# Performance work log

Measured on AMD Instinct MI355X. Metric: run time of the kernel, lower is better.

Reference implementation:

```python
import jax, jax.numpy as jnp
import numpy as np


def _cell(xt, h, c, Wih, Whh, b):
    # Single LSTM cell step; PyTorch gate order i, f, g, o.
    g = xt @ Wih.T + h @ Whh.T + b
    i, f, gg, o = jnp.split(g, 4, axis=-1)
    c = jax.nn.sigmoid(f) * c + jax.nn.sigmoid(i) * jnp.tanh(gg)
    h = jax.nn.sigmoid(o) * jnp.tanh(c)
    return h, c


def _lstm_layer(x, Wih, Whh, b):
    # x: [B, T, D] -> hs: [B, T, H], (h, c): final states [B, H]
    B = x.shape[0]
    H = Whh.shape[1]
    h0 = jnp.zeros((B, H), x.dtype)
    c0 = jnp.zeros((B, H), x.dtype)

    def step(carry, xt):
        h, c = carry
        h, c = _cell(xt, h, c, Wih, Whh, b)
        return (h, c), h

    (h, c), hs = jax.lax.scan(step, (h0, c0), jnp.swapaxes(x, 0, 1))
    return jnp.swapaxes(hs, 0, 1), h, c


def setup_inputs() -> dict:
    key = jax.random.key(0)
    B, T_SRC, D_IN, H, TGT = 512, 256, 32, 128, 64
    ks = iter(jax.random.split(key, 32))
    s_in = 1.0 / np.sqrt(H)

    def u(k, shape):
        return jax.random.uniform(k, shape, jnp.float32, -s_in, s_in)

    inp = {"x": jax.random.normal(next(ks), (B, T_SRC, D_IN), jnp.float32),
           "target_len": TGT}
    for pre in ("enc", "dec"):
        for l, din in ((0, D_IN), (1, H)):
            inp[f"{pre}_Wih{l}"] = u(next(ks), (4 * H, din))
            inp[f"{pre}_Whh{l}"] = u(next(ks), (4 * H, H))
            inp[f"{pre}_bih{l}"] = u(next(ks), (4 * H,))
            inp[f"{pre}_bhh{l}"] = u(next(ks), (4 * H,))
    inp["lin_W"] = u(next(ks), (D_IN, H))
    inp["lin_b"] = u(next(ks), (D_IN,))
    return inp


def reference(x, target_len,
              enc_Wih0, enc_Whh0, enc_bih0, enc_bhh0,
              enc_Wih1, enc_Whh1, enc_bih1, enc_bhh1,
              dec_Wih0, dec_Whh0, dec_bih0, dec_bhh0,
              dec_Wih1, dec_Whh1, dec_bih1, dec_bhh1,
              lin_W, lin_b):
    # --- encoder: 2-layer full-sequence LSTM, zero initial state ---
    hs0, eh0, ec0 = _lstm_layer(x, enc_Wih0, enc_Whh0, enc_bih0 + enc_bhh0)
    _, eh1, ec1 = _lstm_layer(hs0, enc_Wih1, enc_Whh1, enc_bih1 + enc_bhh1)

    # --- decoder: recursive single-step LSTM + linear head, fed back ---
    db0 = dec_bih0 + dec_bhh0
    db1 = dec_bih1 + dec_bhh1
    dec_in0 = x[:, -1, :]  # last source step

    def step(carry, _):
        h0, c0, h1, c1, inp = carry
        h0, c0 = _cell(inp, h0, c0, dec_Wih0, dec_Whh0, db0)
        h1, c1 = _cell(h0, h1, c1, dec_Wih1, dec_Whh1, db1)
        out = h1 @ lin_W.T + lin_b
        return (h0, c0, h1, c1, out), out

    _, outs = jax.lax.scan(step, (eh0, ec0, eh1, ec1, dec_in0), None,
                           length=target_len)
    return jnp.swapaxes(outs, 0, 1)  # [B, target_len, input_size]
```

## Files before the change

kernel.cpp:

```cpp
#include <hip/hip_runtime.h>
#include <cstdint>
#include <cstddef>

typedef short  short8  __attribute__((ext_vector_type(8)));
typedef float  float4v __attribute__((ext_vector_type(4)));

#define MFMA_B16(a,b,c) __builtin_amdgcn_mfma_f32_16x16x32_bf16(a,b,c,0,0,0)

static constexpr int B_  = 512;
static constexpr int T_  = 256;
static constexpr int DIN = 32;
static constexpr int H_  = 128;
static constexpr int TGT = 64;

static constexpr size_t OFF_XFRAG = 0;
static constexpr size_t OFF_EW0   = 8388608;
static constexpr size_t OFF_EW1LO = OFF_EW0   + 163840;
static constexpr size_t OFF_EW1HI = OFF_EW1LO + 131072;
static constexpr size_t OFF_DW0   = OFF_EW1HI + 131072;
static constexpr size_t OFF_DW1LO = OFF_DW0   + 163840;
static constexpr size_t OFF_DW1HI = OFF_DW1LO + 131072;
static constexpr size_t OFF_LIN   = OFF_DW1HI + 131072;
static constexpr size_t OFF_BIAS  = OFF_LIN   + 8192;
static constexpr size_t WS_NEED   = OFF_BIAS  + 8320;

static constexpr int SM_W    = 0;
static constexpr int SM_ABUF = 131072;
static constexpr int SM_INP  = 147712;
static constexpr int SM_LIN  = 148992;
static constexpr int SM_TOTAL= 157184;

__device__ __forceinline__ short f2bf(float f){
  unsigned u = __float_as_uint(f);
  unsigned r = (u + 0x7fffu + ((u>>16)&1u)) >> 16;
  return (short)(r & 0xffffu);
}
__device__ __forceinline__ float fast_sigm(float x){
  float e = __expf(-x);
  return __builtin_amdgcn_rcpf(1.f + e);
}
__device__ __forceinline__ float fast_tanh(float x){
  float e = __expf(-2.f*x);
  return __builtin_amdgcn_rcpf(1.f + e)*2.f - 1.f;
}

__global__ void prep_x_kernel(const float* __restrict__ x, short8* __restrict__ xfrag){
  int i = blockIdx.x*256 + threadIdx.x;
  if (i >= 32*256*64) return;
  int l    = i & 63;
  int t    = (i >> 6) & 255;
  int bblk = i >> 14;
  int b    = bblk*16 + (l & 15);
  const float* src = x + ((size_t)(b*T_ + t))*DIN + ((l>>4)*8);
  short8 v;
  #pragma unroll
  for (int j=0;j<8;j++) v[j] = f2bf(src[j]);
  xfrag[i] = v;
}

__device__ __forceinline__ void pack160(short8* __restrict__ dst,
                                        const float* __restrict__ Wih,
                                        const float* __restrict__ Whh,
                                        int e){
  int nt = e/320; int r = e%320; int kb = r/64; int l = r%64;
  int n  = nt*16 + (l&15);
  short8 v;
  #pragma unroll
  for (int j=0;j<8;j++){
    int k = kb*32 + (l>>4)*8 + j;
    float f = (k < 32) ? Wih[n*32 + k] : Whh[n*128 + (k-32)];
    v[j] = f2bf(f);
  }
  dst[e] = v;
}
__device__ __forceinline__ void pack256s(short8* __restrict__ dlo, short8* __restrict__ dhi,
                                         const float* __restrict__ Wih,
                                         const float* __restrict__ Whh,
                                         int e){
  int nt = e/512; int r = e%512; int kb = r/64; int l = r%64;
  int n  = nt*16 + (l&15);
  short8 v;
  #pragma unroll
  for (int j=0;j<8;j++){
    int k = kb*32 + (l>>4)*8 + j;
    float f = (k < 128) ? Wih[n*128 + k] : Whh[n*128 + (k-128)];
    v[j] = f2bf(f);
  }
  if (kb < 4) dlo[(nt*4 + kb)*64 + l]     = v;
  else        dhi[(nt*4 + (kb-4))*64 + l] = v;
}

__global__ void prep_w_kernel(
    const float* __restrict__ eWih0, const float* __restrict__ eWhh0,
    const float* __restrict__ eWih1, const float* __restrict__ eWhh1,
    const float* __restrict__ dWih0, const float* __restrict__ dWhh0,
    const float* __restrict__ dWih1, const float* __restrict__ dWhh1,
    const float* __restrict__ linW,
    const float* __restrict__ eb0a, const float* __restrict__ eb0b,
    const float* __restrict__ eb1a, const float* __restrict__ eb1b,
    const float* __restrict__ db0a, const float* __restrict__ db0b,
    const float* __restrict__ db1a, const float* __restrict__ db1b,
    const float* __restrict__ linb,
    short8* __restrict__ encW0,
    short8* __restrict__ encW1lo, short8* __restrict__ encW1hi,
    short8* __restrict__ decW0,
    short8* __restrict__ decW1lo, short8* __restrict__ decW1hi,
    short8* __restrict__ linT,  float* __restrict__ biases)
{
  int i = blockIdx.x*256 + threadIdx.x;
  if (i < 10240)       { pack160(encW0, eWih0, eWhh0, i); }
  else if (i < 26624)  { pack256s(encW1lo, encW1hi, eWih1, eWhh1, i-10240); }
  else if (i < 36864)  { pack160(decW0, dWih0, dWhh0, i-26624); }
  else if (i < 53248)  { pack256s(decW1lo, decW1hi, dWih1, dWhh1, i-36864); }
  else if (i < 53760)  {
    int e = i - 53248;
    int nt = e/256; int r = e%256; int kb = r/64; int l = r%64;
    int n = nt*16 + (l&15);
    short8 v;
    #pragma unroll
    for (int j=0;j<8;j++){
      int k = kb*32 + (l>>4)*8 + j;
      v[j] = f2bf(linW[n*128 + k]);
    }
    linT[e] = v;
  }
  else if (i < 55840)  {
    int e = i - 53760;
    float v;
    if      (e < 512)  v = eb0a[e]       + eb0b[e];
    else if (e < 1024) v = eb1a[e-512]   + eb1b[e-512];
    else if (e < 1536) v = db0a[e-1024]  + db0b[e-1024];
    else if (e < 2048) v = db1a[e-1536]  + db1b[e-1536];
    else               v = linb[e-2048];
    biases[e] = v;
  }
}

__global__ __launch_bounds__(512, 1) void lstm_main_kernel(
    const short8* __restrict__ xfrag,
    const short8* __restrict__ encW0,
    const short8* __restrict__ encW1lo, const short8* __restrict__ encW1hi,
    const short8* __restrict__ decW0,
    const short8* __restrict__ decW1lo, const short8* __restrict__ decW1hi,
    const short8* __restrict__ linT,  const float* __restrict__ biases,
    float* __restrict__ out)
{
  extern __shared__ __align__(16) char smem[];
  short8* Wlds        = (short8*)(smem + SM_W);
  short (*Abuf)[520]  = (short(*)[520])(smem + SM_ABUF);
  short (*inpA)[40]   = (short(*)[40])(smem + SM_INP);
  short8* Wlin        = (short8*)(smem + SM_LIN);

  const int tid  = threadIdx.x;
  const int w    = tid >> 6;
  const int l    = tid & 63;
  const int col  = l & 15;
  const int lq   = l >> 4;
  const int bblk = blockIdx.x;

  for (int i = tid; i < 8192; i += 512) Wlds[i] = encW1hi[i];
  for (int i = tid; i < 16*520; i += 512) ((short*)Abuf)[i] = 0;

  short8 W0r[4][5];
  short8 W1lo[4][4];
  #pragma unroll
  for (int i=0;i<4;i++){
    #pragma unroll
    for (int kb=0;kb<5;kb++) W0r[i][kb]  = encW0  [(size_t)(8*i+w)*320 + (size_t)kb*64 + l];
    #pragma unroll
    for (int kb=0;kb<4;kb++) W1lo[i][kb] = encW1lo[(size_t)(8*i+w)*256 + (size_t)kb*64 + l];
  }
  float bs0[4], bs1[4];
  #pragma unroll
  for (int i=0;i<4;i++){
    bs0[i] = biases[       (8*i+w)*16 + col];
    bs1[i] = biases[512 +  (8*i+w)*16 + col];
  }

  float c0[4] = {0.f,0.f,0.f,0.f};
  float c1[4] = {0.f,0.f,0.f,0.f};

  const short8* xf = xfrag + (size_t)bblk*T_*64 + l;
  short8 a0 = xf[0];
  __syncthreads();

  #pragma unroll 2
  for (int t = 0; t < T_; t++){
    const int h0r = (t & 1) * 128;
    const int h0w = 128 - h0r;
    const int h1r = 256 + h0r;
    const int h1w = 256 + h0w;

    short8 ah[4];
    #pragma unroll
    for (int kb=0;kb<4;kb++) ah[kb] = *(const short8*)&Abuf[col][h0r + kb*32 + lq*8];
    float4v acc0[4];
    #pragma unroll
    for (int i=0;i<4;i++){
      float4v a = {bs0[i],bs0[i],bs0[i],bs0[i]};
      a = MFMA_B16(a0, W0r[i][0], a);
      #pragma unroll
      for (int kb=0;kb<4;kb++) a = MFMA_B16(ah[kb], W0r[i][kb+1], a);
      acc0[i] = a;
    }
    short8 a0n = xf[(size_t)((t+1 < T_) ? t+1 : t)*64];
    #pragma unroll
    for (int q=0;q<4;q++){
      float cc = fast_sigm(acc0[1][q])*c0[q] + fast_sigm(acc0[0][q])*fast_tanh(acc0[2][q]);
      c0[q] = cc;
      Abuf[lq*4+q][h0w + 16*w + col] = f2bf(fast_sigm(acc0[3][q])*fast_tanh(cc));
    }
    a0 = a0n;
    __syncthreads();

    short8 a1lo[4], a1hi[4];
    #pragma unroll
    for (int kb=0;kb<4;kb++) a1lo[kb] = *(const short8*)&Abuf[col][h0w + kb*32 + lq*8];
    #pragma unroll
    for (int kb=0;kb<4;kb++) a1hi[kb] = *(const short8*)&Abuf[col][h1r + kb*32 + lq*8];
    float4v acc1[4];
    #pragma unroll
    for (int i=0;i<4;i++){
      float4v a = {bs1[i],bs1[i],bs1[i],bs1[i]};
      #pragma unroll
      for (int kb=0;kb<4;kb++) a = MFMA_B16(a1lo[kb], W1lo[i][kb], a);
      #pragma unroll
      for (int kb=0;kb<4;kb++){
        short8 wv = Wlds[((8*i+w)*4 + kb)*64 + l];
        a = MFMA_B16(a1hi[kb], wv, a);
      }
      acc1[i] = a;
    }
    #pragma unroll
    for (int q=0;q<4;q++){
      float cc = fast_sigm(acc1[1][q])*c1[q] + fast_sigm(acc1[0][q])*fast_tanh(acc1[2][q]);
      c1[q] = cc;
      Abuf[lq*4+q][h1w + 16*w + col] = f2bf(fast_sigm(acc1[3][q])*fast_tanh(cc));
    }
    __syncthreads();
  }

  for (int i = tid; i < 8192; i += 512) Wlds[i] = decW1hi[i];
  if (tid < 512) Wlin[tid] = linT[tid];
  #pragma unroll
  for (int i=0;i<4;i++){
    #pragma unroll
    for (int kb=0;kb<5;kb++) W0r[i][kb]  = decW0  [(size_t)(8*i+w)*320 + (size_t)kb*64 + l];
    #pragma unroll
    for (int kb=0;kb<4;kb++) W1lo[i][kb] = decW1lo[(size_t)(8*i+w)*256 + (size_t)kb*64 + l];
    bs0[i] = biases[1024 + (8*i+w)*16 + col];
    bs1[i] = biases[1536 + (8*i+w)*16 + col];
  }
  float blin = (w < 2) ? biases[2048 + w*16 + col] : 0.f;
  if (w == 0){
    *(short8*)&inpA[col][lq*8] = xf[(size_t)(T_-1)*64];
  }
  __syncthreads();

  #pragma unroll 2
  for (int td = 0; td < TGT; td++){
    const int h0r = (td & 1) * 128;
    const int h0w = 128 - h0r;
    const int h1r = 256 + h0r;
    const int h1w = 256 + h0w;

    short8 a0d = *(const short8*)&inpA[col][lq*8];
    short8 ah[4];
    #pragma unroll
    for (int kb=0;kb<4;kb++) ah[kb] = *(const short8*)&Abuf[col][h0r + kb*32 + lq*8];
    float4v acc0[4];
    #pragma unroll
    for (int i=0;i<4;i++){
      float4v a = {bs0[i],bs0[i],bs0[i],bs0[i]};
      a = MFMA_B16(a0d, W0r[i][0], a);
      #pragma unroll
      for (int kb=0;kb<4;kb++) a = MFMA_B16(ah[kb], W0r[i][kb+1], a);
      acc0[i] = a;
    }
    #pragma unroll
    for (int q=0;q<4;q++){
      float cc = fast_sigm(acc0[1][q])*c0[q] + fast_sigm(acc0[0][q])*fast_tanh(acc0[2][q]);
      c0[q] = cc;
      Abuf[lq*4+q][h0w + 16*w + col] = f2bf(fast_sigm(acc0[3][q])*fast_tanh(cc));
    }
    __syncthreads();

    short8 a1lo[4], a1hi[4];
    #pragma unroll
    for (int kb=0;kb<4;kb++) a1lo[kb] = *(const short8*)&Abuf[col][h0w + kb*32 + lq*8];
    #pragma unroll
    for (int kb=0;kb<4;kb++) a1hi[kb] = *(const short8*)&Abuf[col][h1r + kb*32 + lq*8];
    float4v acc1[4];
    #pragma unroll
    for (int i=0;i<4;i++){
      float4v a = {bs1[i],bs1[i],bs1[i],bs1[i]};
      #pragma unroll
      for (int kb=0;kb<4;kb++) a = MFMA_B16(a1lo[kb], W1lo[i][kb], a);
      #pragma unroll
      for (int kb=0;kb<4;kb++){
        short8 wv = Wlds[((8*i+w)*4 + kb)*64 + l];
        a = MFMA_B16(a1hi[kb], wv, a);
      }
      acc1[i] = a;
    }
    #pragma unroll
    for (int q=0;q<4;q++){
      float cc = fast_sigm(acc1[1][q])*c1[q] + fast_sigm(acc1[0][q])*fast_tanh(acc1[2][q]);
      c1[q] = cc;
      Abuf[lq*4+q][h1w + 16*w + col] = f2bf(fast_sigm(acc1[3][q])*fast_tanh(cc));
    }
    __syncthreads();

    if (w < 2){
      short8 hf[4];
      #pragma unroll
      for (int kb=0;kb<4;kb++) hf[kb] = *(const short8*)&Abuf[col][h1w + kb*32 + lq*8];
      float4v a = {blin,blin,blin,blin};
      #pragma unroll
      for (int kb=0;kb<4;kb++){
        short8 wv = Wlin[(w*4+kb)*64 + l];
        a = MFMA_B16(hf[kb], wv, a);
      }
      #pragma unroll
      for (int q=0;q<4;q++){
        float v = a[q];
        int b = bblk*16 + lq*4 + q;
        out[((size_t)b*TGT + td)*DIN + (w*16 + col)] = v;
        inpA[lq*4+q][w*16 + col] = f2bf(v);
      }
    }
    __syncthreads();
  }
}

extern "C" void kernel_launch(void* const* d_in, const int* in_sizes, int n_in,
                              void* d_out, int out_size, void* d_ws, size_t ws_size,
                              hipStream_t stream) {
  const float* x      = (const float*)d_in[0];
  const float* eWih0  = (const float*)d_in[2];
  const float* eWhh0  = (const float*)d_in[3];
  const float* eb0a   = (const float*)d_in[4];
  const float* eb0b   = (const float*)d_in[5];
  const float* eWih1  = (const float*)d_in[6];
  const float* eWhh1  = (const float*)d_in[7];
  const float* eb1a   = (const float*)d_in[8];
  const float* eb1b   = (const float*)d_in[9];
  const float* dWih0  = (const float*)d_in[10];
  const float* dWhh0  = (const float*)d_in[11];
  const float* db0a   = (const float*)d_in[12];
  const float* db0b   = (const float*)d_in[13];
  const float* dWih1  = (const float*)d_in[14];
  const float* dWhh1  = (const float*)d_in[15];
  const float* db1a   = (const float*)d_in[16];
  const float* db1b   = (const float*)d_in[17];
  const float* linW   = (const float*)d_in[18];
  const float* linb   = (const float*)d_in[19];

  char* ws = (char*)d_ws;
  short8* xfrag   = (short8*)(ws + OFF_XFRAG);
  short8* encW0   = (short8*)(ws + OFF_EW0);
  short8* encW1lo = (short8*)(ws + OFF_EW1LO);
  short8* encW1hi = (short8*)(ws + OFF_EW1HI);
  short8* decW0   = (short8*)(ws + OFF_DW0);
  short8* decW1lo = (short8*)(ws + OFF_DW1LO);
  short8* decW1hi = (short8*)(ws + OFF_DW1HI);
  short8* linT    = (short8*)(ws + OFF_LIN);
  float*  biases  = (float*)(ws + OFF_BIAS);

  hipFuncSetAttribute((const void*)lstm_main_kernel,
                      hipFuncAttributeMaxDynamicSharedMemorySize, SM_TOTAL);

  prep_x_kernel<<<2048, 256, 0, stream>>>(x, xfrag);
  prep_w_kernel<<<219, 256, 0, stream>>>(
      eWih0,eWhh0,eWih1,eWhh1,dWih0,dWhh0,dWih1,dWhh1,linW,
      eb0a,eb0b,eb1a,eb1b,db0a,db0b,db1a,db1b,linb,
      encW0,encW1lo,encW1hi,decW0,decW1lo,decW1hi,linT,biases);
  lstm_main_kernel<<<32, 512, SM_TOTAL, stream>>>(
      xfrag, encW0, encW1lo, encW1hi, decW0, decW1lo, decW1hi,
      linT, biases, (float*)d_out);
}
```

Measured before the change: 745.8 us.

## Software-pipeline encoder layers: run layer1 step t-1 with layer0 step t

Restructures the encoder loop as a wavefront: each iteration computes layer-0 at step i and layer-1 at step i-1 together. Both use the previous layer-0 hidden state already in LDS, so one barrier per timestep replaces two and the two sets of MFMA chains can interleave. A prologue and epilogue handle the first layer-0 and last layer-1 steps, and the decoder's buffer parity is adjusted to match. The cost is higher register pressure from holding both accumulator sets and extra code size.

```diff
diff --git a/kernel.cpp b/kernel.cpp
--- a/kernel.cpp
+++ b/kernel.cpp
@@ -184,58 +184,106 @@
   short8 a0 = xf[0];
   __syncthreads();
 
-  #pragma unroll 2
-  for (int t = 0; t < T_; t++){
-    const int h0r = (t & 1) * 128;
-    const int h0w = 128 - h0r;
-    const int h1r = 256 + h0r;
-    const int h1w = 256 + h0w;
-
-    short8 ah[4];
-    #pragma unroll
-    for (int kb=0;kb<4;kb++) ah[kb] = *(const short8*)&Abuf[col][h0r + kb*32 + lq*8];
+
+  {
+    short8 hp[4];
+    #pragma unroll
+    for (int kb=0;kb<4;kb++) hp[kb] = *(const short8*)&Abuf[col][128 + kb*32 + lq*8];
     float4v acc0[4];
     #pragma unroll
-    for (int i=0;i<4;i++){
-      float4v a = {bs0[i],bs0[i],bs0[i],bs0[i]};
-      a = MFMA_B16(a0, W0r[i][0], a);
-      #pragma unroll
-      for (int kb=0;kb<4;kb++) a = MFMA_B16(ah[kb], W0r[i][kb+1], a);
-      acc0[i] = a;
-    }
-    short8 a0n = xf[(size_t)((t+1 < T_) ? t+1 : t)*64];
+    for (int i4=0;i4<4;i4++){
+      float4v a = {bs0[i4],bs0[i4],bs0[i4],bs0[i4]};
+      a = MFMA_B16(a0, W0r[i4][0], a);
+      #pragma unroll
+      for (int kb=0;kb<4;kb++) a = MFMA_B16(hp[kb], W0r[i4][kb+1], a);
+      acc0[i4] = a;
+    }
+    a0 = xf[64];
     #pragma unroll
     for (int q=0;q<4;q++){
       float cc = fast_sigm(acc0[1][q])*c0[q] + fast_sigm(acc0[0][q])*fast_tanh(acc0[2][q]);
       c0[q] = cc;
-      Abuf[lq*4+q][h0w + 16*w + col] = f2bf(fast_sigm(acc0[3][q])*fast_tanh(cc));
-    }
-    a0 = a0n;
-    __syncthreads();
-
-    short8 a1lo[4], a1hi[4];
-    #pragma unroll
-    for (int kb=0;kb<4;kb++) a1lo[kb] = *(const short8*)&Abuf[col][h0w + kb*32 + lq*8];
-    #pragma unroll
-    for (int kb=0;kb<4;kb++) a1hi[kb] = *(const short8*)&Abuf[col][h1r + kb*32 + lq*8];
-    float4v acc1[4];
-    #pragma unroll
-    for (int i=0;i<4;i++){
-      float4v a = {bs1[i],bs1[i],bs1[i],bs1[i]};
-      #pragma unroll
-      for (int kb=0;kb<4;kb++) a = MFMA_B16(a1lo[kb], W1lo[i][kb], a);
+      Abuf[lq*4+q][0 + 16*w + col] = f2bf(fast_sigm(acc0[3][q])*fast_tanh(cc));
+    }
+    __syncthreads();
+  }
+
+  #pragma unroll 2
+  for (int i = 1; i < T_; i++){
+    const int p_h0_r = ((i-1)&1)*128;
+    const int p_h0_w = (i&1)*128;
+    const int p_h1_r = 256 + (i&1)*128;
+    const int p_h1_w = 256 + ((i-1)&1)*128;
+
+    short8 hp[4], h1p[4];
+    #pragma unroll
+    for (int kb=0;kb<4;kb++) hp[kb]  = *(const short8*)&Abuf[col][p_h0_r + kb*32 + lq*8];
+    #pragma unroll
+    for (int kb=0;kb<4;kb++) h1p[kb] = *(const short8*)&Abuf[col][p_h1_r + kb*32 + lq*8];
+
+    float4v acc0[4], acc1[4];
+    #pragma unroll
+    for (int i4=0;i4<4;i4++){
+      float4v a = {bs0[i4],bs0[i4],bs0[i4],bs0[i4]};
+      a = MFMA_B16(a0, W0r[i4][0], a);
+      #pragma unroll
+      for (int kb=0;kb<4;kb++) a = MFMA_B16(hp[kb], W0r[i4][kb+1], a);
+      acc0[i4] = a;
+
+      float4v b = {bs1[i4],bs1[i4],bs1[i4],bs1[i4]};
+      #pragma unroll
+      for (int kb=0;kb<4;kb++) b = MFMA_B16(hp[kb], W1lo[i4][kb], b);
       #pragma unroll
       for (int kb=0;kb<4;kb++){
-        short8 wv = Wlds[((8*i+w)*4 + kb)*64 + l];
-        a = MFMA_B16(a1hi[kb], wv, a);
+        short8 wv = Wlds[((8*i4+w)*4 + kb)*64 + l];
+        b = MFMA_B16(h1p[kb], wv, b);
       }
-      acc1[i] = a;
+      acc1[i4] = b;
+    }
+    a0 = xf[(size_t)((i+1 < T_) ? i+1 : i)*64];
+
+    #pragma unroll
+    for (int q=0;q<4;q++){
+      float cc = fast_sigm(acc0[1][q])*c0[q] + fast_sigm(acc0[0][q])*fast_tanh(acc0[2][q]);
+      c0[q] = cc;
+      Abuf[lq*4+q][p_h0_w + 16*w + col] = f2bf(fast_sigm(acc0[3][q])*fast_tanh(cc));
     }
     #pragma unroll
     for (int q=0;q<4;q++){
       float cc = fast_sigm(acc1[1][q])*c1[q] + fast_sigm(acc1[0][q])*fast_tanh(acc1[2][q]);
       c1[q] = cc;
-      Abuf[lq*4+q][h1w + 16*w + col] = f2bf(fast_sigm(acc1[3][q])*fast_tanh(cc));
+      Abuf[lq*4+q][p_h1_w + 16*w + col] = f2bf(fast_sigm(acc1[3][q])*fast_tanh(cc));
+    }
+    __syncthreads();
+  }
+
+  {
+    const int p_h0_r = 128;
+    const int p_h1_r = 256 + 0;
+    const int p_h1_w = 256 + 128;
+    short8 hp[4], h1p[4];
+    #pragma unroll
+    for (int kb=0;kb<4;kb++) hp[kb]  = *(const short8*)&Abuf[col][p_h0_r + kb*32 + lq*8];
+    #pragma unroll
+    for (int kb=0;kb<4;kb++) h1p[kb] = *(const short8*)&Abuf[col][p_h1_r + kb*32 + lq*8];
+    float4v acc1[4];
+    #pragma unroll
+    for (int i4=0;i4<4;i4++){
+      float4v b = {bs1[i4],bs1[i4],bs1[i4],bs1[i4]};
+      #pragma unroll
+      for (int kb=0;kb<4;kb++) b = MFMA_B16(hp[kb], W1lo[i4][kb], b);
+      #pragma unroll
+      for (int kb=0;kb<4;kb++){
+        short8 wv = Wlds[((8*i4+w)*4 + kb)*64 + l];
+        b = MFMA_B16(h1p[kb], wv, b);
+      }
+      acc1[i4] = b;
+    }
+    #pragma unroll
+    for (int q=0;q<4;q++){
+      float cc = fast_sigm(acc1[1][q])*c1[q] + fast_sigm(acc1[0][q])*fast_tanh(acc1[2][q]);
+      c1[q] = cc;
+      Abuf[lq*4+q][p_h1_w + 16*w + col] = f2bf(fast_sigm(acc1[3][q])*fast_tanh(cc));
     }
     __syncthreads();
   }
@@ -259,7 +307,7 @@
 
   #pragma unroll 2
   for (int td = 0; td < TGT; td++){
-    const int h0r = (td & 1) * 128;
+    const int h0r = ((td+1)&1) * 128;
     const int h0w = 128 - h0r;
     const int h1r = 256 + h0r;
     const int h1w = 256 + h0w;
```

Measured after the change: 736.6 us. Within noise of the previous version (-1.2%).
